# Optimization experiments

Hardware: AMD Instinct MI355X
Metric: run time of the kernel (lower is better)

## Reference

```python
import jax, jax.numpy as jnp
import numpy as np
from math import pi as PI, log

B, N, D, K = 16, 16384, 64, 64


def setup_inputs() -> dict:
    key = jax.random.key(0)
    k1, k2, k3, k4 = jax.random.split(key, 4)
    x = jax.random.normal(k1, (B, N, D), dtype=jnp.float32)
    pi_w = jax.nn.softmax(jax.random.normal(k2, (K,), dtype=jnp.float32))  # mixture weights, sum to 1
    mu = jax.random.normal(k3, (K, D), dtype=jnp.float32)
    var = jax.random.uniform(k4, (K, D), dtype=jnp.float32, minval=0.5, maxval=1.5)  # diagonal variances
    return {"x": x, "pi": pi_w, "mu": mu, "var": var}


def reference(x, pi, mu, var):
    b, n, d = x.shape
    # --- gmm.predict_proba: diagonal-covariance Gaussian log-likelihoods + log pi, softmax over K ---
    inv_var = 1.0 / var                                   # (K, D)
    x2 = x * x                                            # (B, N, D)
    # Mahalanobis distance expanded via matmuls to avoid a (B,N,K,D) intermediate
    maha = (jnp.einsum('bnd,kd->bnk', x2, inv_var)
            - 2.0 * jnp.einsum('bnd,kd->bnk', x, mu * inv_var)
            + jnp.sum(mu * mu * inv_var, axis=-1))        # (B, N, K)
    log_det = jnp.sum(jnp.log(var), axis=-1)              # (K,)
    log_prob = -0.5 * (d * log(2.0 * PI) + log_det + maha)
    Q = jax.nn.softmax(log_prob + jnp.log(pi), axis=-1)   # (B, N, K) responsibilities
    # --- weighted reductions over N ---
    Q_sum = jnp.sum(Q, axis=1) / n                         # (B, K)
    Q_x = jnp.einsum('bnk,bnd->bkd', Q, x) / n             # (B, K, D)
    Q_x2 = jnp.einsum('bnk,bnd->bkd', Q, x2) / n           # (B, K, D)
    # --- Fisher-vector statistics ---
    d_pi = Q_sum - pi                                      # (B, K)
    qs = Q_sum[..., None]                                  # (B, K, 1)
    d_mu = Q_x - qs * mu
    d_sigma = -Q_x2 - qs * (mu * mu) + qs * var + 2.0 * Q_x * mu
    return jnp.concatenate([d_pi.reshape(b, -1), d_mu.reshape(b, -1), d_sigma.reshape(b, -1)], axis=1)
```

## Files before the change

kernel.cpp:

```cpp
#include <hip/hip_runtime.h>
#include <hip/hip_bf16.h>
#include <math.h>

#define B_  16
#define N_  16384
#define D_  64
#define K_  64
#define OUT_PER_B (K_ + 2*K_*D_)
#define CHUNKS 32
#define NTILES (N_ / CHUNKS / 64)

#define WS_C0_OFF   4096
#define WS_PART_OFF 4160
#define PART_STRIDE (64*4 + 2*4096*2)

typedef float f32x4 __attribute__((ext_vector_type(4)));
typedef short short8 __attribute__((ext_vector_type(8)));

union U8 { short8 s8; unsigned int u[4]; };

__device__ __forceinline__ unsigned short f2bf(float f) {
    union { float f; unsigned int u; } v; v.f = f;
    unsigned int r = v.u + 0x7FFFu + ((v.u >> 16) & 1u);
    return (unsigned short)(r >> 16);
}

__device__ __forceinline__ unsigned int f2bf2(float lo, float hi) {
    __hip_bfloat162 h = __float22bfloat162_rn(make_float2(lo, hi));
    unsigned int u;
    __builtin_memcpy(&u, &h, 4);
    return u;
}

__device__ __forceinline__ float bf2f(unsigned short u) {
    unsigned int v = ((unsigned int)u) << 16;
    float f;
    __builtin_memcpy(&f, &v, 4);
    return f;
}

__global__ __launch_bounds__(256) void fv_prep(const float* __restrict__ pi,
                                               const float* __restrict__ mu,
                                               const float* __restrict__ var,
                                               float* __restrict__ ws) {
    __shared__ float red[256];
    int t = threadIdx.x;
    unsigned short* wt = (unsigned short*)ws;
    for (int i = t; i < 4096; i += 256) {
        int k = i >> 6, d = i & 63;
        float v  = var[i];
        float m  = mu[i];
        float iv = 1.0f / v;
        wt[k * 128 + d]      = f2bf(-0.5f * iv);
        wt[k * 128 + 64 + d] = f2bf(m * iv);
    }
    int k = t >> 2, pr = t & 3;
    float s = 0.0f;
    #pragma unroll
    for (int j = 0; j < 16; ++j) {
        int d = pr * 16 + j;
        float v = var[k * 64 + d];
        float m = mu[k * 64 + d];
        s += __logf(v) + m * m / v;
    }
    red[t] = s;
    __syncthreads();
    if (pr == 0) {
        float sum = red[4 * k] + red[4 * k + 1] + red[4 * k + 2] + red[4 * k + 3];
        ws[WS_C0_OFF + k] = __logf(pi[k]) - 0.5f * (117.6241322502f + sum);
    }
}

__global__ __launch_bounds__(256, 2) void fv_main(const float* __restrict__ x,
                                                  const float* __restrict__ ws,
                                                  char* __restrict__ partials) {
    __shared__ __align__(16) unsigned short QtS[2][64 * 72];
    __shared__ float qsum_s[4][64];

    const int t    = threadIdx.x;
    const int w    = t >> 6;
    const int lane = t & 63;
    const int r16  = lane & 15;
    const int q    = lane >> 4;

    short8 wfrag[4][4];
    f32x4  c0v[4];
    {
        const unsigned short* wsu = (const unsigned short*)ws;
        #pragma unroll
        for (int kt = 0; kt < 4; ++kt) {
            const unsigned short* wr = wsu + (16 * kt + r16) * 128 + 8 * q;
            #pragma unroll
            for (int h = 0; h < 4; ++h)
                wfrag[kt][h] = *(const short8*)(const void*)(wr + 32 * h);
            c0v[kt] = *(const f32x4*)(ws + WS_C0_OFF + 16 * kt + 4 * q);
        }
    }

    const int bi    = blockIdx.y;
    const int chunk = blockIdx.x;
    const int ppb   = N_ / CHUNKS;
    const float* xb = x + ((size_t)bi * N_ + (size_t)chunk * ppb) * D_;

    f32x4 accX[4]  = {};
    f32x4 accX2[4] = {};
    float qsacc[4][4] = {};

    const int rowoff = (16 * w + r16) * D_ + 8 * q;
    const int dcol   = 16 * w + r16;

    float4 va, vb, vc, vd;
    {
        const float* xr = xb + rowoff;
        va = *(const float4*)(xr);
        vb = *(const float4*)(xr + 4);
        vc = *(const float4*)(xr + 32);
        vd = *(const float4*)(xr + 36);
    }

    #pragma unroll 2
    for (int tile = 0; tile < NTILES; ++tile) {
        const float* xt = xb + (size_t)tile * 64 * D_;

        float4 nva, nvb, nvc, nvd;
        if (tile + 1 < NTILES) {
            const float* xr = xt + 64 * D_ + rowoff;
            nva = *(const float4*)(xr);
            nvb = *(const float4*)(xr + 4);
            nvc = *(const float4*)(xr + 32);
            nvd = *(const float4*)(xr + 36);
        }

        U8 fxa, fxb, fx2a, fx2b;
        fxa.u[0]  = f2bf2(va.x, va.y);           fxa.u[1]  = f2bf2(va.z, va.w);
        fxa.u[2]  = f2bf2(vb.x, vb.y);           fxa.u[3]  = f2bf2(vb.z, vb.w);
        fxb.u[0]  = f2bf2(vc.x, vc.y);           fxb.u[1]  = f2bf2(vc.z, vc.w);
        fxb.u[2]  = f2bf2(vd.x, vd.y);           fxb.u[3]  = f2bf2(vd.z, vd.w);
        fx2a.u[0] = f2bf2(va.x*va.x, va.y*va.y); fx2a.u[1] = f2bf2(va.z*va.z, va.w*va.w);
        fx2a.u[2] = f2bf2(vb.x*vb.x, vb.y*vb.y); fx2a.u[3] = f2bf2(vb.z*vb.z, vb.w*vb.w);
        fx2b.u[0] = f2bf2(vc.x*vc.x, vc.y*vc.y); fx2b.u[1] = f2bf2(vc.z*vc.z, vc.w*vc.w);
        fx2b.u[2] = f2bf2(vd.x*vd.x, vd.y*vd.y); fx2b.u[3] = f2bf2(vd.z*vd.z, vd.w*vd.w);

        float sc[4][4];
        #pragma unroll
        for (int kt = 0; kt < 4; ++kt) {
            f32x4 a = c0v[kt];
            a = __builtin_amdgcn_mfma_f32_16x16x32_bf16(wfrag[kt][0], fx2a.s8, a, 0, 0, 0);
            a = __builtin_amdgcn_mfma_f32_16x16x32_bf16(wfrag[kt][1], fx2b.s8, a, 0, 0, 0);
            a = __builtin_amdgcn_mfma_f32_16x16x32_bf16(wfrag[kt][2], fxa.s8,  a, 0, 0, 0);
            a = __builtin_amdgcn_mfma_f32_16x16x32_bf16(wfrag[kt][3], fxb.s8,  a, 0, 0, 0);
            sc[kt][0] = a[0]; sc[kt][1] = a[1]; sc[kt][2] = a[2]; sc[kt][3] = a[3];
        }

        float mx = sc[0][0];
        #pragma unroll
        for (int kt = 0; kt < 4; ++kt)
            #pragma unroll
            for (int rr = 0; rr < 4; ++rr) mx = fmaxf(mx, sc[kt][rr]);
        mx = fmaxf(mx, __shfl_xor(mx, 16));
        mx = fmaxf(mx, __shfl_xor(mx, 32));
        float z = 0.0f;
        #pragma unroll
        for (int kt = 0; kt < 4; ++kt)
            #pragma unroll
            for (int rr = 0; rr < 4; ++rr) {
                sc[kt][rr] = __expf(sc[kt][rr] - mx);
                z += sc[kt][rr];
            }
        z += __shfl_xor(z, 16);
        z += __shfl_xor(z, 32);
        float inv = 1.0f / z;
        const int p = 16 * w + r16;
        unsigned short* Qb = QtS[tile & 1];
        #pragma unroll
        for (int kt = 0; kt < 4; ++kt) {
            #pragma unroll
            for (int rr = 0; rr < 4; rr += 2) {
                float q0 = sc[kt][rr] * inv;
                float q1 = sc[kt][rr + 1] * inv;
                qsacc[kt][rr]     += q0;
                qsacc[kt][rr + 1] += q1;
                unsigned int pk = f2bf2(q0, q1);
                Qb[(16 * kt + 4 * q + rr)     * 72 + p] = (unsigned short)pk;
                Qb[(16 * kt + 4 * q + rr + 1) * 72 + p] = (unsigned short)(pk >> 16);
            }
        }

        float vle[16];
        {
            const float* xc = xt + dcol;
            #pragma unroll
            for (int c = 0; c < 2; ++c)
                #pragma unroll
                for (int j = 0; j < 8; ++j)
                    vle[8 * c + j] = xc[(32 * c + 8 * q + j) * D_];
        }

        asm volatile("s_waitcnt lgkmcnt(0)\n\ts_barrier" ::: "memory");

        U8 fxp0, fxp1, fx2p0, fx2p1;
        #pragma unroll
        for (int i = 0; i < 4; ++i) {
            float a0 = vle[2 * i], a1 = vle[2 * i + 1];
            float b0 = vle[8 + 2 * i], b1 = vle[8 + 2 * i + 1];
            fxp0.u[i]  = f2bf2(a0, a1);
            fxp1.u[i]  = f2bf2(b0, b1);
            fx2p0.u[i] = f2bf2(a0 * a0, a1 * a1);
            fx2p1.u[i] = f2bf2(b0 * b0, b1 * b1);
        }
        #pragma unroll
        for (int kt = 0; kt < 4; ++kt) {
            const unsigned short* qr = &Qb[(16 * kt + r16) * 72 + 8 * q];
            short8 aq0 = *(const short8*)(const void*)(qr);
            short8 aq1 = *(const short8*)(const void*)(qr + 32);
            accX[kt]  = __builtin_amdgcn_mfma_f32_16x16x32_bf16(aq0, fxp0.s8,  accX[kt],  0, 0, 0);
            accX2[kt] = __builtin_amdgcn_mfma_f32_16x16x32_bf16(aq0, fx2p0.s8, accX2[kt], 0, 0, 0);
            accX[kt]  = __builtin_amdgcn_mfma_f32_16x16x32_bf16(aq1, fxp1.s8,  accX[kt],  0, 0, 0);
            accX2[kt] = __builtin_amdgcn_mfma_f32_16x16x32_bf16(aq1, fx2p1.s8, accX2[kt], 0, 0, 0);
        }

        va = nva; vb = nvb; vc = nvc; vd = nvd;
    }

    char* rec = partials + ((size_t)bi * CHUNKS + chunk) * PART_STRIDE;
    float* part_qs = (float*)rec;
    unsigned short* part_qx  = (unsigned short*)(rec + 256);
    unsigned short* part_qx2 = part_qx + 4096;
    #pragma unroll
    for (int kt = 0; kt < 4; ++kt)
        #pragma unroll
        for (int rr = 0; rr < 4; ++rr) {
            int k = 16 * kt + 4 * q + rr;
            part_qx [k * 64 + 16 * w + r16] = f2bf(accX[kt][rr]);
            part_qx2[k * 64 + 16 * w + r16] = f2bf(accX2[kt][rr]);
        }
    #pragma unroll
    for (int kt = 0; kt < 4; ++kt)
        #pragma unroll
        for (int rr = 0; rr < 4; ++rr) {
            float v = qsacc[kt][rr];
            v += __shfl_xor(v, 1);
            v += __shfl_xor(v, 2);
            v += __shfl_xor(v, 4);
            v += __shfl_xor(v, 8);
            if (r16 == 0) qsum_s[w][16 * kt + 4 * q + rr] = v;
        }
    __syncthreads();
    if (t < 64)
        part_qs[t] = qsum_s[0][t] + qsum_s[1][t] + qsum_s[2][t] + qsum_s[3][t];
}

__global__ __launch_bounds__(256) void fv_finalize(const float* __restrict__ pi,
                                                   const float* __restrict__ mu,
                                                   const float* __restrict__ var,
                                                   const char* __restrict__ partials,
                                                   float* __restrict__ out) {
    int g = blockIdx.x * 256 + threadIdx.x;
    if (g >= B_ * OUT_PER_B) return;
    int b   = g / OUT_PER_B;
    int pos = g - b * OUT_PER_B;
    const char* base = partials + (size_t)b * CHUNKS * PART_STRIDE;
    const float invN = 1.0f / (float)N_;

    if (pos < 64) {
        float qs = 0.0f;
        for (int c = 0; c < CHUNKS; ++c)
            qs += ((const float*)(base + c * PART_STRIDE))[pos];
        out[g] = qs * invN - pi[pos];
    } else if (pos < 64 + 4096) {
        int idx = pos - 64;
        int k = idx >> 6;
        float qs = 0.0f, qx = 0.0f;
        for (int c = 0; c < CHUNKS; ++c) {
            const char* r = base + c * PART_STRIDE;
            qs += ((const float*)r)[k];
            qx += bf2f(((const unsigned short*)(r + 256))[idx]);
        }
        out[g] = (qx - qs * mu[idx]) * invN;
    } else {
        int idx = pos - 64 - 4096;
        int k = idx >> 6;
        float qs = 0.0f, qx = 0.0f, qx2 = 0.0f;
        for (int c = 0; c < CHUNKS; ++c) {
            const char* r = base + c * PART_STRIDE;
            qs  += ((const float*)r)[k];
            qx  += bf2f(((const unsigned short*)(r + 256))[idx]);
            qx2 += bf2f(((const unsigned short*)(r + 256))[4096 + idx]);
        }
        float m = mu[idx], v = var[idx];
        out[g] = (-qx2 - qs * m * m + qs * v + 2.0f * qx * m) * invN;
    }
}

extern "C" void kernel_launch(void* const* d_in, const int* in_sizes, int n_in,
                              void* d_out, int out_size, void* d_ws, size_t ws_size,
                              hipStream_t stream) {
    const float* x   = (const float*)d_in[0];
    const float* pi  = (const float*)d_in[1];
    const float* mu  = (const float*)d_in[2];
    const float* var = (const float*)d_in[3];
    float* ws = (float*)d_ws;
    char* partials = (char*)(ws + WS_PART_OFF);

    fv_prep<<<1, 256, 0, stream>>>(pi, mu, var, ws);
    fv_main<<<dim3(CHUNKS, B_), 256, 0, stream>>>(x, ws, partials);
    int total = B_ * OUT_PER_B;
    fv_finalize<<<(total + 255) / 256, 256, 0, stream>>>(pi, mu, var, partials,
                                                         (float*)d_out);
}
```

Baseline: 120.6 us.

## Stage GMM weight fragments in LDS to cut registers and raise occupancy

Moves the bf16 weight matrix and constant offsets out of per-thread registers into shared memory, reading the fragments from LDS on each tile. This frees about 64 VGPRs so launch bounds can target 3 blocks per CU. It also doubles the N chunking so there are twice as many blocks. The cost is extra LDS reads in the inner loop, more shared memory per block, and more partials to reduce.

```diff
diff --git a/kernel.cpp b/kernel.cpp
--- a/kernel.cpp
+++ b/kernel.cpp
@@ -7,7 +7,7 @@
 #define D_  64
 #define K_  64
 #define OUT_PER_B (K_ + 2*K_*D_)
-#define CHUNKS 32
+#define CHUNKS 64
 #define NTILES (N_ / CHUNKS / 64)
 
 #define WS_C0_OFF   4096
@@ -71,9 +71,11 @@
     }
 }
 
-__global__ __launch_bounds__(256, 2) void fv_main(const float* __restrict__ x,
+__global__ __launch_bounds__(256, 3) void fv_main(const float* __restrict__ x,
                                                   const float* __restrict__ ws,
                                                   char* __restrict__ partials) {
+    __shared__ __align__(16) unsigned short WtS[64 * 136];
+    __shared__ float c0s[64];
     __shared__ __align__(16) unsigned short QtS[2][64 * 72];
     __shared__ float qsum_s[4][64];
 
@@ -83,18 +85,13 @@
     const int r16  = lane & 15;
     const int q    = lane >> 4;
 
-    short8 wfrag[4][4];
-    f32x4  c0v[4];
     {
-        const unsigned short* wsu = (const unsigned short*)ws;
-        #pragma unroll
-        for (int kt = 0; kt < 4; ++kt) {
-            const unsigned short* wr = wsu + (16 * kt + r16) * 128 + 8 * q;
-            #pragma unroll
-            for (int h = 0; h < 4; ++h)
-                wfrag[kt][h] = *(const short8*)(const void*)(wr + 32 * h);
-            c0v[kt] = *(const f32x4*)(ws + WS_C0_OFF + 16 * kt + 4 * q);
-        }
+        const uint4* src = (const uint4*)ws;
+        for (int i = t; i < 1024; i += 256) {
+            int row = i >> 4, u = i & 15;
+            *(uint4*)&WtS[row * 136 + u * 8] = src[i];
+        }
+        if (t < 64) c0s[t] = ws[WS_C0_OFF + t];
     }
 
     const int bi    = blockIdx.y;
@@ -117,6 +114,8 @@
         vc = *(const float4*)(xr + 32);
         vd = *(const float4*)(xr + 36);
     }
+
+    __syncthreads();
 
     #pragma unroll 2
     for (int tile = 0; tile < NTILES; ++tile) {
@@ -144,11 +143,16 @@
         float sc[4][4];
         #pragma unroll
         for (int kt = 0; kt < 4; ++kt) {
-            f32x4 a = c0v[kt];
-            a = __builtin_amdgcn_mfma_f32_16x16x32_bf16(wfrag[kt][0], fx2a.s8, a, 0, 0, 0);
-            a = __builtin_amdgcn_mfma_f32_16x16x32_bf16(wfrag[kt][1], fx2b.s8, a, 0, 0, 0);
-            a = __builtin_amdgcn_mfma_f32_16x16x32_bf16(wfrag[kt][2], fxa.s8,  a, 0, 0, 0);
-            a = __builtin_amdgcn_mfma_f32_16x16x32_bf16(wfrag[kt][3], fxb.s8,  a, 0, 0, 0);
+            const unsigned short* wr = &WtS[(16 * kt + r16) * 136 + 8 * q];
+            short8 w0 = *(const short8*)(const void*)(wr);
+            short8 w1 = *(const short8*)(const void*)(wr + 32);
+            short8 w2 = *(const short8*)(const void*)(wr + 64);
+            short8 w3 = *(const short8*)(const void*)(wr + 96);
+            f32x4 a = *(const f32x4*)&c0s[16 * kt + 4 * q];
+            a = __builtin_amdgcn_mfma_f32_16x16x32_bf16(w0, fx2a.s8, a, 0, 0, 0);
+            a = __builtin_amdgcn_mfma_f32_16x16x32_bf16(w1, fx2b.s8, a, 0, 0, 0);
+            a = __builtin_amdgcn_mfma_f32_16x16x32_bf16(w2, fxa.s8,  a, 0, 0, 0);
+            a = __builtin_amdgcn_mfma_f32_16x16x32_bf16(w3, fxb.s8,  a, 0, 0, 0);
             sc[kt][0] = a[0]; sc[kt][1] = a[1]; sc[kt][2] = a[2]; sc[kt][3] = a[3];
         }
 
```

Measured after the change: 128.5 us. 1.07x slower.

## Fuse GMM parameter prep into main kernel and hoist column x loads

Applied to the files above, without the earlier changes.

Removes the separate single-block prep kernel. Each main-kernel block now computes its bf16 weight fragments (-0.5/var, mu/var) and the per-component constant terms directly from mu, var and pi, using shared memory and two block barriers. This drops one kernel launch and the serialization it forces between prep and main, but every block repeats the parameter math. The strided per-column x loads are also moved to the top of each tile iteration, so their latency overlaps with the softmax and Q-store work.

```diff
diff --git a/kernel.cpp b/kernel.cpp
--- a/kernel.cpp
+++ b/kernel.cpp
@@ -10,8 +10,6 @@
 #define CHUNKS 32
 #define NTILES (N_ / CHUNKS / 64)
 
-#define WS_C0_OFF   4096
-#define WS_PART_OFF 4160
 #define PART_STRIDE (64*4 + 2*4096*2)
 
 typedef float f32x4 __attribute__((ext_vector_type(4)));
@@ -39,43 +37,15 @@
     return f;
 }
 
-__global__ __launch_bounds__(256) void fv_prep(const float* __restrict__ pi,
-                                               const float* __restrict__ mu,
-                                               const float* __restrict__ var,
-                                               float* __restrict__ ws) {
-    __shared__ float red[256];
-    int t = threadIdx.x;
-    unsigned short* wt = (unsigned short*)ws;
-    for (int i = t; i < 4096; i += 256) {
-        int k = i >> 6, d = i & 63;
-        float v  = var[i];
-        float m  = mu[i];
-        float iv = 1.0f / v;
-        wt[k * 128 + d]      = f2bf(-0.5f * iv);
-        wt[k * 128 + 64 + d] = f2bf(m * iv);
-    }
-    int k = t >> 2, pr = t & 3;
-    float s = 0.0f;
-    #pragma unroll
-    for (int j = 0; j < 16; ++j) {
-        int d = pr * 16 + j;
-        float v = var[k * 64 + d];
-        float m = mu[k * 64 + d];
-        s += __logf(v) + m * m / v;
-    }
-    red[t] = s;
-    __syncthreads();
-    if (pr == 0) {
-        float sum = red[4 * k] + red[4 * k + 1] + red[4 * k + 2] + red[4 * k + 3];
-        ws[WS_C0_OFF + k] = __logf(pi[k]) - 0.5f * (117.6241322502f + sum);
-    }
-}
-
 __global__ __launch_bounds__(256, 2) void fv_main(const float* __restrict__ x,
-                                                  const float* __restrict__ ws,
+                                                  const float* __restrict__ pi,
+                                                  const float* __restrict__ mu,
+                                                  const float* __restrict__ var,
                                                   char* __restrict__ partials) {
     __shared__ __align__(16) unsigned short QtS[2][64 * 72];
     __shared__ float qsum_s[4][64];
+    __shared__ float red[256];
+    __shared__ float c0s[64];
 
     const int t    = threadIdx.x;
     const int w    = t >> 6;
@@ -83,19 +53,61 @@
     const int r16  = lane & 15;
     const int q    = lane >> 4;
 
+    {
+        int k = t >> 2, pr = t & 3;
+        float s = 0.0f;
+        #pragma unroll
+        for (int j = 0; j < 16; ++j) {
+            int d = pr * 16 + j;
+            float v = var[k * 64 + d];
+            float m = mu[k * 64 + d];
+            s += __logf(v) + m * m / v;
+        }
+        red[t] = s;
+    }
+
     short8 wfrag[4][4];
-    f32x4  c0v[4];
-    {
-        const unsigned short* wsu = (const unsigned short*)ws;
-        #pragma unroll
-        for (int kt = 0; kt < 4; ++kt) {
-            const unsigned short* wr = wsu + (16 * kt + r16) * 128 + 8 * q;
-            #pragma unroll
-            for (int h = 0; h < 4; ++h)
-                wfrag[kt][h] = *(const short8*)(const void*)(wr + 32 * h);
-            c0v[kt] = *(const f32x4*)(ws + WS_C0_OFF + 16 * kt + 4 * q);
-        }
-    }
+    #pragma unroll
+    for (int kt = 0; kt < 4; ++kt) {
+        const int k = 16 * kt + r16;
+        const float* vr = var + k * 64 + 8 * q;
+        const float* mr = mu  + k * 64 + 8 * q;
+        float vv[16], mm[16];
+        *(float4*)&vv[0]  = *(const float4*)(vr);
+        *(float4*)&vv[4]  = *(const float4*)(vr + 4);
+        *(float4*)&vv[8]  = *(const float4*)(vr + 32);
+        *(float4*)&vv[12] = *(const float4*)(vr + 36);
+        *(float4*)&mm[0]  = *(const float4*)(mr);
+        *(float4*)&mm[4]  = *(const float4*)(mr + 4);
+        *(float4*)&mm[8]  = *(const float4*)(mr + 32);
+        *(float4*)&mm[12] = *(const float4*)(mr + 36);
+        float iv[16];
+        #pragma unroll
+        for (int i = 0; i < 16; ++i) iv[i] = 1.0f / vv[i];
+        U8 h0, h1, h2, h3;
+        #pragma unroll
+        for (int i = 0; i < 4; ++i) {
+            h0.u[i] = f2bf2(-0.5f * iv[2*i],     -0.5f * iv[2*i + 1]);
+            h1.u[i] = f2bf2(-0.5f * iv[8 + 2*i], -0.5f * iv[8 + 2*i + 1]);
+            h2.u[i] = f2bf2(mm[2*i] * iv[2*i],   mm[2*i+1] * iv[2*i + 1]);
+            h3.u[i] = f2bf2(mm[8+2*i] * iv[8+2*i], mm[8+2*i+1] * iv[8+2*i+1]);
+        }
+        wfrag[kt][0] = h0.s8; wfrag[kt][1] = h1.s8;
+        wfrag[kt][2] = h2.s8; wfrag[kt][3] = h3.s8;
+    }
+
+    __syncthreads();
+    if ((t & 3) == 0) {
+        int k = t >> 2;
+        float sum = red[4 * k] + red[4 * k + 1] + red[4 * k + 2] + red[4 * k + 3];
+        c0s[k] = __logf(pi[k]) - 0.5f * (117.6241322502f + sum);
+    }
+    __syncthreads();
+
+    f32x4 c0v[4];
+    #pragma unroll
+    for (int kt = 0; kt < 4; ++kt)
+        c0v[kt] = *(const f32x4*)&c0s[16 * kt + 4 * q];
 
     const int bi    = blockIdx.y;
     const int chunk = blockIdx.x;
@@ -121,6 +133,16 @@
     #pragma unroll 2
     for (int tile = 0; tile < NTILES; ++tile) {
         const float* xt = xb + (size_t)tile * 64 * D_;
+
+        float vle[16];
+        {
+            const float* xc = xt + dcol;
+            #pragma unroll
+            for (int c = 0; c < 2; ++c)
+                #pragma unroll
+                for (int j = 0; j < 8; ++j)
+                    vle[8 * c + j] = xc[(32 * c + 8 * q + j) * D_];
+        }
 
         float4 nva, nvb, nvc, nvd;
         if (tile + 1 < NTILES) {
@@ -184,16 +206,6 @@
                 Qb[(16 * kt + 4 * q + rr)     * 72 + p] = (unsigned short)pk;
                 Qb[(16 * kt + 4 * q + rr + 1) * 72 + p] = (unsigned short)(pk >> 16);
             }
-        }
-
-        float vle[16];
-        {
-            const float* xc = xt + dcol;
-            #pragma unroll
-            for (int c = 0; c < 2; ++c)
-                #pragma unroll
-                for (int j = 0; j < 8; ++j)
-                    vle[8 * c + j] = xc[(32 * c + 8 * q + j) * D_];
         }
 
         asm volatile("s_waitcnt lgkmcnt(0)\n\ts_barrier" ::: "memory");
@@ -299,11 +311,9 @@
     const float* pi  = (const float*)d_in[1];
     const float* mu  = (const float*)d_in[2];
     const float* var = (const float*)d_in[3];
-    float* ws = (float*)d_ws;
-    char* partials = (char*)(ws + WS_PART_OFF);
-
-    fv_prep<<<1, 256, 0, stream>>>(pi, mu, var, ws);
-    fv_main<<<dim3(CHUNKS, B_), 256, 0, stream>>>(x, ws, partials);
+    char* partials = (char*)d_ws;
+
+    fv_main<<<dim3(CHUNKS, B_), 256, 0, stream>>>(x, pi, mu, var, partials);
     int total = B_ * OUT_PER_B;
     fv_finalize<<<(total + 255) / 256, 256, 0, stream>>>(pi, mu, var, partials,
                                                          (float*)d_out);
```

After: 120.0 us (median of 2 runs). No clear change (-0.5%).
